# Kernel optimization log

Measured on AMD Instinct MI355X. Metric: run time of the kernel, lower is better.

The kernel has to match this reference:

```python
import jax, jax.numpy as jnp
import numpy as np

B, C, T, H, HI = 256, 64, 512, 8, 3


def setup_inputs() -> dict:
    key = jax.random.key(0)
    ks = jax.random.split(key, 20)
    s = 0.1
    return {
        "x": jax.random.normal(ks[0], (B, C, T), jnp.float32),
        "m": jax.random.uniform(ks[1], (B, C, T), jnp.float32),
        "d": jax.random.uniform(ks[2], (B, C, T), jnp.float32),
        # interpolater params (per-channel blocks of the block-diagonal matrices)
        "Wf": jax.random.normal(ks[3], (C, H, H), jnp.float32) * s,
        "Vf": jax.random.normal(ks[4], (C, H, 3), jnp.float32) * s,
        "cf": jax.random.normal(ks[5], (C, H), jnp.float32) * s,
        "Wb": jax.random.normal(ks[6], (C, H, H), jnp.float32) * s,
        "Vb": jax.random.normal(ks[7], (C, H, 3), jnp.float32) * s,
        "cb": jax.random.normal(ks[8], (C, H), jnp.float32) * s,
        "U": jax.random.normal(ks[9], (C, 2 * H), jnp.float32) * s,
        "c0": jax.random.normal(ks[10], (C,), jnp.float32) * s,
        # imputer params (nn.Linear: y = x @ W.T + b)
        "V1_w": jax.random.normal(ks[11], (HI, C), jnp.float32) * s,
        "V2_w": jax.random.normal(ks[12], (HI, C), jnp.float32) * s,
        "U_w": jax.random.normal(ks[13], (HI, C), jnp.float32) * s,
        "U_b": jax.random.normal(ks[14], (HI,), jnp.float32) * s,
        "W_w": jax.random.normal(ks[15], (C, HI), jnp.float32) * s,
        "W_b": jax.random.normal(ks[16], (C,), jnp.float32) * s,
    }


def _mrnn_forward(x, m, d, Wf, Vf, cf, Wb, Vb, cb, U, c0,
                  V1_w, V2_w, U_w, U_b, W_w, W_b):
    act = jax.nn.relu
    Bv, Cv, Tv = x.shape
    Hv = Wf.shape[-1]
    # replication pad along time: [B,C,T] -> [B,C,T+2]
    pad = lambda a: jnp.pad(a, ((0, 0), (0, 0), (1, 1)), mode='edge')
    s = jnp.stack([pad(x), pad(m), pad(d)], axis=-1)        # [B,C,T+2,3]
    # forward scan consumes padded times 0..T-1; backward consumes T+1 down to 2
    in_f = jnp.moveaxis(s[:, :, :Tv], 2, 0)                 # [T,B,C,3]
    in_b = jnp.moveaxis(s[:, :, 2:Tv + 2][:, :, ::-1], 2, 0)  # [T,B,C,3]

    def make_step(W, V, c):
        def step(h, inp):  # h:[B,C,H] inp:[B,C,3]
            hn = act(jnp.einsum('chk,bck->bch', W, h)
                     + jnp.einsum('chj,bcj->bch', V, inp) + c)
            return hn, hn
        return step

    h0 = jnp.zeros((Bv, Cv, Hv), x.dtype)
    _, hf = jax.lax.scan(make_step(Wf, Vf, cf), h0, in_f)   # [T,B,C,H]
    _, hb = jax.lax.scan(make_step(Wb, Vb, cb), h0, in_b)
    hb = hb[::-1]  # align backward hiddens with time index

    x_est = act(jnp.einsum('ch,tbch->bct', U[:, :Hv], hf)
                + jnp.einsum('ch,tbch->bct', U[:, Hv:], hb)
                + c0[None, :, None])                        # [B,C,T]

    # imputer (time as batch dim); U weight has zeroed diagonal
    idx = jnp.arange(min(U_w.shape[0], Cv))
    Uz = U_w.at[idx, idx].set(0.0)
    h = act(jnp.swapaxes(x_est, 1, 2) @ V1_w.T
            + jnp.swapaxes(m, 1, 2) @ V2_w.T
            + jnp.swapaxes(x, 1, 2) @ Uz.T + U_b)           # [B,T,HI]
    out = h @ W_w.T + W_b                                   # [B,T,C]
    return jnp.swapaxes(out, 1, 2)                          # [B,C,T]


def reference(x, m, d, Wf, Vf, cf, Wb, Vb, cb, U, c0,
              V1_w, V2_w, U_w, U_b, W_w, W_b):
    return _mrnn_forward(x, m, d, Wf, Vf, cf, Wb, Vb, cb, U, c0,
                         V1_w, V2_w, U_w, U_b, W_w, W_b)
```

## Files before the change

kernel.cpp:

```cpp
#include <hip/hip_runtime.h>

constexpr int Tn = 512;
constexpr int Cn = 64;
constexpr int Bn = 256;
constexpr int NS = 16384;

typedef float f2 __attribute__((ext_vector_type(2)));

template<int CTRL>
__device__ __forceinline__ float dppf(float v) {
    int i = __builtin_bit_cast(int, v);
    i = __builtin_amdgcn_mov_dpp(i, CTRL, 0xF, 0xF, true);
    return __builtin_bit_cast(float, i);
}

#define LDLINE(XB, MB, DB, U0) do {                                         \
    const float4* _px = (const float4*)(xp + (U0));                         \
    const float4* _pm = (const float4*)(mp + (U0));                         \
    const float4* _pd = (const float4*)(dp + (U0));                         \
    _Pragma("unroll")                                                       \
    for (int q = 0; q < 4; ++q) {                                           \
        float4 v;                                                           \
        v = _px[q]; XB[4*q]=v.x; XB[4*q+1]=v.y; XB[4*q+2]=v.z; XB[4*q+3]=v.w; \
        v = _pm[q]; MB[4*q]=v.x; MB[4*q+1]=v.y; MB[4*q+2]=v.z; MB[4*q+3]=v.w; \
        v = _pd[q]; DB[4*q]=v.x; DB[4*q+1]=v.y; DB[4*q+2]=v.z; DB[4*q+3]=v.w; \
    }                                                                       \
} while (0)

#define RUNF(XB, MB, DB, N) do {                                            \
    _Pragma("unroll")                                                       \
    for (int k = 0; k < (N); ++k) { *op = step(XB[k], MB[k], DB[k]); op += NS; } \
} while (0)

#define RUNB(XB, MB, DB, N) do {                                            \
    _Pragma("unroll")                                                       \
    for (int k = 0; k < (N); ++k) { *op = step(XB[15-k], MB[15-k], DB[15-k]); op -= NS; } \
} while (0)

__global__ __launch_bounds__(256, 2) void mrnn_scan(
    const float* __restrict__ x, const float* __restrict__ m, const float* __restrict__ d,
    const float* __restrict__ Wf, const float* __restrict__ Vf, const float* __restrict__ cf,
    const float* __restrict__ Wb, const float* __restrict__ Vb, const float* __restrict__ cbk,
    const float* __restrict__ U, float* __restrict__ accF, float* __restrict__ accB)
{
    const int g   = blockIdx.x * blockDim.x + threadIdx.x;
    const int q   = g & 3;
    const int sd  = g >> 2;
    const int dir = sd >> 14;
    const int seq = sd & 16383;
    const int c   = seq & 63;
    const long base = (long)seq * Tn;

    const float* W  = dir ? Wb  : Wf;
    const float* V  = dir ? Vb  : Vf;
    const float* cc = dir ? cbk : cf;

    const int r0 = 2 * q;
    const int r1 = 2 * q + 1;

    f2 Wp[8], Vp[3], cbp, Up;
    #pragma unroll
    for (int k = 0; k < 8; ++k) {
        Wp[k].x = W[c*64 + r0*8 + k];
        Wp[k].y = W[c*64 + r1*8 + k];
    }
    #pragma unroll
    for (int k = 0; k < 3; ++k) {
        Vp[k].x = V[c*24 + r0*3 + k];
        Vp[k].y = V[c*24 + r1*3 + k];
    }
    cbp.x = cc[c*8 + r0];  cbp.y = cc[c*8 + r1];
    Up.x  = U[c*16 + dir*8 + r0];
    Up.y  = U[c*16 + dir*8 + r1];

    f2 h = {0.f, 0.f};
    const float* xp = x + base;
    const float* mp = m + base;
    const float* dp = d + base;
    float* op = (dir ? accB : accF) + seq;

    auto step = [&](float xv, float mv, float dv) -> float {
        const float h0 = dppf<0x00>(h.x), h1 = dppf<0x00>(h.y);
        const float h2 = dppf<0x55>(h.x), h3 = dppf<0x55>(h.y);
        const float h4 = dppf<0xAA>(h.x), h5 = dppf<0xAA>(h.y);
        const float h6 = dppf<0xFF>(h.x), h7 = dppf<0xFF>(h.y);
        f2 acc = cbp;
        acc += Vp[0] * xv;
        acc += Vp[1] * mv;
        acc += Vp[2] * dv;
        acc += Wp[0] * h0;  acc += Wp[1] * h1;
        acc += Wp[2] * h2;  acc += Wp[3] * h3;
        acc += Wp[4] * h4;  acc += Wp[5] * h5;
        acc += Wp[6] * h6;  acc += Wp[7] * h7;
        acc.x = fmaxf(acc.x, 0.f);
        acc.y = fmaxf(acc.y, 0.f);
        h = acc;
        f2 dp2 = Up * acc;
        float pd = dp2.x + dp2.y;
        pd += dppf<0xB1>(pd);
        pd += dppf<0x4E>(pd);
        return pd;
    };

    float ax[16], am[16], ad[16], bx[16], bm[16], bd[16];

    if (dir == 0) {
        LDLINE(ax, am, ad, 0);
        LDLINE(bx, bm, bd, 16);
        *op = step(ax[0], am[0], ad[0]); op += NS;
        #pragma unroll 1
        for (int i = 0; i < 15; ++i) {
            RUNF(ax, am, ad, 16);
            LDLINE(ax, am, ad, 32*i + 32);
            RUNF(bx, bm, bd, 16);
            LDLINE(bx, bm, bd, 32*i + 48);
        }
        RUNF(ax, am, ad, 16);
        RUNF(bx, bm, bd, 15);
    } else {
        op += 511 * NS;
        LDLINE(ax, am, ad, 496);
        LDLINE(bx, bm, bd, 480);
        *op = step(ax[15], am[15], ad[15]); op -= NS;
        #pragma unroll 1
        for (int i = 0; i < 15; ++i) {
            RUNB(ax, am, ad, 16);
            LDLINE(ax, am, ad, 16*(29 - 2*i));
            RUNB(bx, bm, bd, 16);
            LDLINE(bx, bm, bd, 16*(28 - 2*i));
        }
        RUNB(ax, am, ad, 16);
        RUNB(bx, bm, bd, 15);
    }
}

__global__ __launch_bounds__(256, 2) void mrnn_mix(
    const float* __restrict__ x, const float* __restrict__ m,
    const float* __restrict__ accF, const float* __restrict__ accB,
    const float* __restrict__ c0, const float* __restrict__ V1w,
    const float* __restrict__ V2w, const float* __restrict__ Uw,
    const float* __restrict__ Ub, const float* __restrict__ Ww,
    const float* __restrict__ Wbias, float* __restrict__ out)
{
    const int bt = blockIdx.x * 256 + threadIdx.x;
    const int b = bt >> 9;
    const int t = bt & 511;

    const float4* aF4 = (const float4*)(accF + (size_t)t * NS + b * Cn);
    const float4* aB4 = (const float4*)(accB + (size_t)t * NS + b * Cn);
    const size_t xb = (size_t)b * (Cn * Tn) + t;

    float h0 = Ub[0], h1 = Ub[1], h2 = Ub[2];
    #pragma unroll
    for (int c4 = 0; c4 < 16; ++c4) {
        const float4 fa = aF4[c4];
        const float4 fb = aB4[c4];
        const float fav[4] = {fa.x, fa.y, fa.z, fa.w};
        const float fbv[4] = {fb.x, fb.y, fb.z, fb.w};
        #pragma unroll
        for (int j = 0; j < 4; ++j) {
            const int cch = 4*c4 + j;
            const float xe = fmaxf(fav[j] + fbv[j] + c0[cch], 0.f);
            const float mv = m[xb + (size_t)cch * Tn];
            const float xv = x[xb + (size_t)cch * Tn];
            const float u0 = (cch == 0) ? 0.f : Uw[0*Cn + cch];
            const float u1 = (cch == 1) ? 0.f : Uw[1*Cn + cch];
            const float u2 = (cch == 2) ? 0.f : Uw[2*Cn + cch];
            h0 += V1w[0*Cn + cch]*xe + V2w[0*Cn + cch]*mv + u0*xv;
            h1 += V1w[1*Cn + cch]*xe + V2w[1*Cn + cch]*mv + u1*xv;
            h2 += V1w[2*Cn + cch]*xe + V2w[2*Cn + cch]*mv + u2*xv;
        }
    }
    h0 = fmaxf(h0, 0.f); h1 = fmaxf(h1, 0.f); h2 = fmaxf(h2, 0.f);

    float* opt = out + (size_t)b * (Cn * Tn) + t;
    #pragma unroll
    for (int cch = 0; cch < Cn; ++cch) {
        opt[(size_t)cch * Tn] = Wbias[cch] + Ww[cch*3 + 0]*h0 + Ww[cch*3 + 1]*h1 + Ww[cch*3 + 2]*h2;
    }
}

extern "C" void kernel_launch(void* const* d_in, const int* in_sizes, int n_in,
                              void* d_out, int out_size, void* d_ws, size_t ws_size,
                              hipStream_t stream)
{
    const float* x   = (const float*)d_in[0];
    const float* m   = (const float*)d_in[1];
    const float* d   = (const float*)d_in[2];
    const float* Wf  = (const float*)d_in[3];
    const float* Vf  = (const float*)d_in[4];
    const float* cf  = (const float*)d_in[5];
    const float* Wb  = (const float*)d_in[6];
    const float* Vb  = (const float*)d_in[7];
    const float* cb  = (const float*)d_in[8];
    const float* U   = (const float*)d_in[9];
    const float* c0  = (const float*)d_in[10];
    const float* V1w = (const float*)d_in[11];
    const float* V2w = (const float*)d_in[12];
    const float* Uw  = (const float*)d_in[13];
    const float* Ub  = (const float*)d_in[14];
    const float* Ww  = (const float*)d_in[15];
    const float* Wb_ = (const float*)d_in[16];
    float* out = (float*)d_out;

    float* accF = (float*)d_ws;
    float* accB = accF + (size_t)Tn * NS;

    mrnn_scan<<<512, 256, 0, stream>>>(x, m, d, Wf, Vf, cf, Wb, Vb, cb, U, accF, accB);
    mrnn_mix<<<512, 256, 0, stream>>>(x, m, accF, accB, c0, V1w, V2w, Uw, Ub, Ww, Wb_, out);
}
```

Measured before the change: 114.2 us.

## Use rotating DPP broadcast and split accumulators in scan recurrence

Each quad lane now gathers the hidden state by rotating it through the quad with a single DPP rotate, three rotations per step, instead of eight separate broadcast DPP moves. The weight columns are pre-permuted per lane to match the rotation order. Two accumulator chains shorten the dependent FMA chain on the serial critical path. The input prefetch is also restructured from 16-wide register buffers to float4 double-buffering with a carried element, which cuts register pressure but shortens the prefetch distance.

```diff
diff --git a/kernel.cpp b/kernel.cpp
--- a/kernel.cpp
+++ b/kernel.cpp
@@ -2,7 +2,6 @@
 
 constexpr int Tn = 512;
 constexpr int Cn = 64;
-constexpr int Bn = 256;
 constexpr int NS = 16384;
 
 typedef float f2 __attribute__((ext_vector_type(2)));
@@ -13,28 +12,46 @@
     i = __builtin_amdgcn_mov_dpp(i, CTRL, 0xF, 0xF, true);
     return __builtin_bit_cast(float, i);
 }
-
-#define LDLINE(XB, MB, DB, U0) do {                                         \
-    const float4* _px = (const float4*)(xp + (U0));                         \
-    const float4* _pm = (const float4*)(mp + (U0));                         \
-    const float4* _pd = (const float4*)(dp + (U0));                         \
-    _Pragma("unroll")                                                       \
-    for (int q = 0; q < 4; ++q) {                                           \
-        float4 v;                                                           \
-        v = _px[q]; XB[4*q]=v.x; XB[4*q+1]=v.y; XB[4*q+2]=v.z; XB[4*q+3]=v.w; \
-        v = _pm[q]; MB[4*q]=v.x; MB[4*q+1]=v.y; MB[4*q+2]=v.z; MB[4*q+3]=v.w; \
-        v = _pd[q]; DB[4*q]=v.x; DB[4*q+1]=v.y; DB[4*q+2]=v.z; DB[4*q+3]=v.w; \
-    }                                                                       \
+__device__ __forceinline__ f2 rot1(f2 v) {
+    f2 r; r.x = dppf<0x39>(v.x); r.y = dppf<0x39>(v.y); return r;
+}
+
+#define QSTEP(xv, mv, dv, SGN) do {                                   \
+    f2 hr = h;                                                        \
+    f2 a0 = cbp + Vp0 * (xv);                                         \
+    f2 a1 = Vp1 * (mv);                                               \
+    a0 += Vp2 * (dv);                                                 \
+    a0 += WA0 * hr.x;  a1 += WB0 * hr.y;                              \
+    hr = rot1(hr);                                                    \
+    a0 += WA1 * hr.x;  a1 += WB1 * hr.y;                              \
+    hr = rot1(hr);                                                    \
+    a0 += WA2 * hr.x;  a1 += WB2 * hr.y;                              \
+    hr = rot1(hr);                                                    \
+    a0 += WA3 * hr.x;  a1 += WB3 * hr.y;                              \
+    f2 hn = a0 + a1;                                                  \
+    hn.x = fmaxf(hn.x, 0.f); hn.y = fmaxf(hn.y, 0.f);                 \
+    h = hn;                                                           \
+    float pdv = Up.x * hn.x + Up.y * hn.y;                            \
+    pdv += dppf<0xB1>(pdv);                                           \
+    pdv += dppf<0x4E>(pdv);                                           \
+    *op = pdv;                                                        \
+    op SGN NS;                                                        \
 } while (0)
 
-#define RUNF(XB, MB, DB, N) do {                                            \
-    _Pragma("unroll")                                                       \
-    for (int k = 0; k < (N); ++k) { *op = step(XB[k], MB[k], DB[k]); op += NS; } \
+#define GRP_F(X4, M4, D4) do {                                        \
+    QSTEP(cx, cm, cd, +=);                                            \
+    QSTEP((X4).x, (M4).x, (D4).x, +=);                                \
+    QSTEP((X4).y, (M4).y, (D4).y, +=);                                \
+    QSTEP((X4).z, (M4).z, (D4).z, +=);                                \
+    cx = (X4).w; cm = (M4).w; cd = (D4).w;                            \
 } while (0)
 
-#define RUNB(XB, MB, DB, N) do {                                            \
-    _Pragma("unroll")                                                       \
-    for (int k = 0; k < (N); ++k) { *op = step(XB[15-k], MB[15-k], DB[15-k]); op -= NS; } \
+#define GRP_B(X4, M4, D4) do {                                        \
+    QSTEP(cx, cm, cd, -=);                                            \
+    QSTEP((X4).w, (M4).w, (D4).w, -=);                                \
+    QSTEP((X4).z, (M4).z, (D4).z, -=);                                \
+    QSTEP((X4).y, (M4).y, (D4).y, -=);                                \
+    cx = (X4).x; cm = (M4).x; cd = (D4).x;                            \
 } while (0)
 
 __global__ __launch_bounds__(256, 2) void mrnn_scan(
@@ -55,82 +72,69 @@
     const float* V  = dir ? Vb  : Vf;
     const float* cc = dir ? cbk : cf;
 
-    const int r0 = 2 * q;
-    const int r1 = 2 * q + 1;
-
-    f2 Wp[8], Vp[3], cbp, Up;
-    #pragma unroll
-    for (int k = 0; k < 8; ++k) {
-        Wp[k].x = W[c*64 + r0*8 + k];
-        Wp[k].y = W[c*64 + r1*8 + k];
-    }
-    #pragma unroll
-    for (int k = 0; k < 3; ++k) {
-        Vp[k].x = V[c*24 + r0*3 + k];
-        Vp[k].y = V[c*24 + r1*3 + k];
-    }
-    cbp.x = cc[c*8 + r0];  cbp.y = cc[c*8 + r1];
-    Up.x  = U[c*16 + dir*8 + r0];
-    Up.y  = U[c*16 + dir*8 + r1];
+    const int r0 = 2*q, r1 = 2*q + 1;
+
+    f2 WA0, WA1, WA2, WA3, WB0, WB1, WB2, WB3, Vp0, Vp1, Vp2, cbp, Up;
+    {
+        const float* Wc = W + c*64;
+        int col;
+        col = 2*((q+0)&3);
+        WA0 = f2{Wc[r0*8+col],   Wc[r1*8+col]};
+        WB0 = f2{Wc[r0*8+col+1], Wc[r1*8+col+1]};
+        col = 2*((q+1)&3);
+        WA1 = f2{Wc[r0*8+col],   Wc[r1*8+col]};
+        WB1 = f2{Wc[r0*8+col+1], Wc[r1*8+col+1]};
+        col = 2*((q+2)&3);
+        WA2 = f2{Wc[r0*8+col],   Wc[r1*8+col]};
+        WB2 = f2{Wc[r0*8+col+1], Wc[r1*8+col+1]};
+        col = 2*((q+3)&3);
+        WA3 = f2{Wc[r0*8+col],   Wc[r1*8+col]};
+        WB3 = f2{Wc[r0*8+col+1], Wc[r1*8+col+1]};
+    }
+    Vp0 = f2{V[c*24 + r0*3 + 0], V[c*24 + r1*3 + 0]};
+    Vp1 = f2{V[c*24 + r0*3 + 1], V[c*24 + r1*3 + 1]};
+    Vp2 = f2{V[c*24 + r0*3 + 2], V[c*24 + r1*3 + 2]};
+    cbp = f2{cc[c*8 + r0], cc[c*8 + r1]};
+    Up  = f2{U[c*16 + dir*8 + r0], U[c*16 + dir*8 + r1]};
 
     f2 h = {0.f, 0.f};
-    const float* xp = x + base;
-    const float* mp = m + base;
-    const float* dp = d + base;
+    float cx, cm, cd;
+    const float4* x4 = (const float4*)(x + base);
+    const float4* m4 = (const float4*)(m + base);
+    const float4* d4 = (const float4*)(d + base);
     float* op = (dir ? accB : accF) + seq;
 
-    auto step = [&](float xv, float mv, float dv) -> float {
-        const float h0 = dppf<0x00>(h.x), h1 = dppf<0x00>(h.y);
-        const float h2 = dppf<0x55>(h.x), h3 = dppf<0x55>(h.y);
-        const float h4 = dppf<0xAA>(h.x), h5 = dppf<0xAA>(h.y);
-        const float h6 = dppf<0xFF>(h.x), h7 = dppf<0xFF>(h.y);
-        f2 acc = cbp;
-        acc += Vp[0] * xv;
-        acc += Vp[1] * mv;
-        acc += Vp[2] * dv;
-        acc += Wp[0] * h0;  acc += Wp[1] * h1;
-        acc += Wp[2] * h2;  acc += Wp[3] * h3;
-        acc += Wp[4] * h4;  acc += Wp[5] * h5;
-        acc += Wp[6] * h6;  acc += Wp[7] * h7;
-        acc.x = fmaxf(acc.x, 0.f);
-        acc.y = fmaxf(acc.y, 0.f);
-        h = acc;
-        f2 dp2 = Up * acc;
-        float pd = dp2.x + dp2.y;
-        pd += dppf<0xB1>(pd);
-        pd += dppf<0x4E>(pd);
-        return pd;
-    };
-
-    float ax[16], am[16], ad[16], bx[16], bm[16], bd[16];
-
     if (dir == 0) {
-        LDLINE(ax, am, ad, 0);
-        LDLINE(bx, bm, bd, 16);
-        *op = step(ax[0], am[0], ad[0]); op += NS;
+        float4 Ax = x4[0], Am = m4[0], Ad = d4[0];
+        float4 Bx = x4[1], Bm = m4[1], Bd = d4[1];
+        cx = Ax.x; cm = Am.x; cd = Ad.x;
         #pragma unroll 1
-        for (int i = 0; i < 15; ++i) {
-            RUNF(ax, am, ad, 16);
-            LDLINE(ax, am, ad, 32*i + 32);
-            RUNF(bx, bm, bd, 16);
-            LDLINE(bx, bm, bd, 32*i + 48);
+        for (int i = 0; i < 63; ++i) {
+            float4 Txq = x4[2*i+2], Tmq = m4[2*i+2], Tdq = d4[2*i+2];
+            GRP_F(Ax, Am, Ad);
+            float4 Uxq = x4[2*i+3], Umq = m4[2*i+3], Udq = d4[2*i+3];
+            GRP_F(Bx, Bm, Bd);
+            Ax = Txq; Am = Tmq; Ad = Tdq;
+            Bx = Uxq; Bm = Umq; Bd = Udq;
         }
-        RUNF(ax, am, ad, 16);
-        RUNF(bx, bm, bd, 15);
+        GRP_F(Ax, Am, Ad);
+        GRP_F(Bx, Bm, Bd);
     } else {
         op += 511 * NS;
-        LDLINE(ax, am, ad, 496);
-        LDLINE(bx, bm, bd, 480);
-        *op = step(ax[15], am[15], ad[15]); op -= NS;
+        float4 Ax = x4[127], Am = m4[127], Ad = d4[127];
+        float4 Bx = x4[126], Bm = m4[126], Bd = d4[126];
+        cx = Ax.w; cm = Am.w; cd = Ad.w;
         #pragma unroll 1
-        for (int i = 0; i < 15; ++i) {
-            RUNB(ax, am, ad, 16);
-            LDLINE(ax, am, ad, 16*(29 - 2*i));
-            RUNB(bx, bm, bd, 16);
-            LDLINE(bx, bm, bd, 16*(28 - 2*i));
+        for (int i = 0; i < 63; ++i) {
+            float4 Txq = x4[125-2*i], Tmq = m4[125-2*i], Tdq = d4[125-2*i];
+            GRP_B(Ax, Am, Ad);
+            float4 Uxq = x4[124-2*i], Umq = m4[124-2*i], Udq = d4[124-2*i];
+            GRP_B(Bx, Bm, Bd);
+            Ax = Txq; Am = Tmq; Ad = Tdq;
+            Bx = Uxq; Bm = Umq; Bd = Udq;
         }
-        RUNB(ax, am, ad, 16);
-        RUNB(bx, bm, bd, 15);
+        GRP_B(Ax, Am, Ad);
+        GRP_B(Bx, Bm, Bd);
     }
 }
 
```

Measured after the change: 116.8 us. 2.3% more time.

## Compute RNN recurrence steps with bf16 MFMA instead of DPP FMAs

Applied to the files above, without the earlier changes.

Each wavefront now handles 16 batch sequences for one channel and direction. Every time step becomes a single 16x16x32 bf16 MFMA, with W, V and the bias packed into the A fragment and the hidden state plus inputs packed into the B fragment. The projected outputs are stored as float4 groups of four timesteps in a new [T/4][C][B][4] workspace layout, and the mix kernel is adapted to read that layout. This is meant to cut per-step VALU and DPP work, but converting the hidden state to bf16 adds rounding error that compounds across the recurrence, and 3/4 of the matrix unit's capacity is wasted.

```diff
diff --git a/kernel.cpp b/kernel.cpp
--- a/kernel.cpp
+++ b/kernel.cpp
@@ -2,135 +2,163 @@
 
 constexpr int Tn = 512;
 constexpr int Cn = 64;
-constexpr int Bn = 256;
 constexpr int NS = 16384;
 
-typedef float f2 __attribute__((ext_vector_type(2)));
-
-template<int CTRL>
-__device__ __forceinline__ float dppf(float v) {
+typedef __attribute__((ext_vector_type(8))) short short8;
+typedef __attribute__((ext_vector_type(4))) float f32x4;
+typedef __attribute__((ext_vector_type(4))) int   i32x4;
+
+__device__ __forceinline__ unsigned cvt_pk_bf16(float lo, float hi) {
+    unsigned r;
+    asm("v_cvt_pk_bf16_f32 %0, %1, %2" : "=v"(r) : "v"(lo), "v"(hi));
+    return r;
+}
+__device__ __forceinline__ float swz_xor16(float v) {
     int i = __builtin_bit_cast(int, v);
-    i = __builtin_amdgcn_mov_dpp(i, CTRL, 0xF, 0xF, true);
+    i = __builtin_amdgcn_ds_swizzle(i, 0x401F);
     return __builtin_bit_cast(float, i);
 }
 
-#define LDLINE(XB, MB, DB, U0) do {                                         \
-    const float4* _px = (const float4*)(xp + (U0));                         \
-    const float4* _pm = (const float4*)(mp + (U0));                         \
-    const float4* _pd = (const float4*)(dp + (U0));                         \
-    _Pragma("unroll")                                                       \
-    for (int q = 0; q < 4; ++q) {                                           \
-        float4 v;                                                           \
-        v = _px[q]; XB[4*q]=v.x; XB[4*q+1]=v.y; XB[4*q+2]=v.z; XB[4*q+3]=v.w; \
-        v = _pm[q]; MB[4*q]=v.x; MB[4*q+1]=v.y; MB[4*q+2]=v.z; MB[4*q+3]=v.w; \
-        v = _pd[q]; DB[4*q]=v.x; DB[4*q+1]=v.y; DB[4*q+2]=v.z; DB[4*q+3]=v.w; \
-    }                                                                       \
+#define GRP_F(X4, M4, P4) do {                                        \
+    v0 = step(cx, cm, cd);                                            \
+    v1 = step((X4).x, (M4).x, (P4).x);                                \
+    v2 = step((X4).y, (M4).y, (P4).y);                                \
+    v3 = step((X4).z, (M4).z, (P4).z);                                \
+    if (doSt) *(float4*)op = make_float4(v0, v1, v2, v3);             \
+    op += 65536;                                                      \
+    cx = (X4).w; cm = (M4).w; cd = (P4).w;                            \
 } while (0)
 
-#define RUNF(XB, MB, DB, N) do {                                            \
-    _Pragma("unroll")                                                       \
-    for (int k = 0; k < (N); ++k) { *op = step(XB[k], MB[k], DB[k]); op += NS; } \
-} while (0)
-
-#define RUNB(XB, MB, DB, N) do {                                            \
-    _Pragma("unroll")                                                       \
-    for (int k = 0; k < (N); ++k) { *op = step(XB[15-k], MB[15-k], DB[15-k]); op -= NS; } \
+#define GRP_B(X4, M4, P4) do {                                        \
+    v3 = step(cx, cm, cd);                                            \
+    v2 = step((X4).w, (M4).w, (P4).w);                                \
+    v1 = step((X4).z, (M4).z, (P4).z);                                \
+    v0 = step((X4).y, (M4).y, (P4).y);                                \
+    if (doSt) *(float4*)op = make_float4(v0, v1, v2, v3);             \
+    op -= 65536;                                                      \
+    cx = (X4).x; cm = (M4).x; cd = (P4).x;                            \
 } while (0)
 
 __global__ __launch_bounds__(256, 2) void mrnn_scan(
     const float* __restrict__ x, const float* __restrict__ m, const float* __restrict__ d,
     const float* __restrict__ Wf, const float* __restrict__ Vf, const float* __restrict__ cf,
     const float* __restrict__ Wb, const float* __restrict__ Vb, const float* __restrict__ cbk,
-    const float* __restrict__ U, float* __restrict__ accF, float* __restrict__ accB)
+    const float* __restrict__ Uu, float* __restrict__ accF, float* __restrict__ accB)
 {
-    const int g   = blockIdx.x * blockDim.x + threadIdx.x;
-    const int q   = g & 3;
-    const int sd  = g >> 2;
-    const int dir = sd >> 14;
-    const int seq = sd & 16383;
-    const int c   = seq & 63;
-    const long base = (long)seq * Tn;
+    const int w    = blockIdx.x * 4 + (threadIdx.x >> 6);
+    const int bg   = w & 15;
+    const int c    = (w >> 4) & 63;
+    const int dir  = w >> 10;
+    const int lane = threadIdx.x & 63;
+    const int col  = lane & 15;
+    const int grp  = lane >> 4;
+    const int b    = bg * 16 + col;
 
     const float* W  = dir ? Wb  : Wf;
     const float* V  = dir ? Vb  : Vf;
     const float* cc = dir ? cbk : cf;
 
-    const int r0 = 2 * q;
-    const int r1 = 2 * q + 1;
-
-    f2 Wp[8], Vp[3], cbp, Up;
-    #pragma unroll
-    for (int k = 0; k < 8; ++k) {
-        Wp[k].x = W[c*64 + r0*8 + k];
-        Wp[k].y = W[c*64 + r1*8 + k];
-    }
-    #pragma unroll
-    for (int k = 0; k < 3; ++k) {
-        Vp[k].x = V[c*24 + r0*3 + k];
-        Vp[k].y = V[c*24 + r1*3 + k];
-    }
-    cbp.x = cc[c*8 + r0];  cbp.y = cc[c*8 + r1];
-    Up.x  = U[c*16 + dir*8 + r0];
-    Up.y  = U[c*16 + dir*8 + r1];
-
-    f2 h = {0.f, 0.f};
-    const float* xp = x + base;
-    const float* mp = m + base;
-    const float* dp = d + base;
-    float* op = (dir ? accB : accF) + seq;
+    float a0 = 0.f, a1 = 0.f, a2 = 0.f, a3 = 0.f;
+    {
+        const int row = col;
+        if (row < 8) {
+            if (grp == 0) {
+                const float* Wc = W + c*64 + row*8;
+                a0 = Wc[0]; a1 = Wc[1]; a2 = Wc[2]; a3 = Wc[3];
+            } else if (grp == 1) {
+                const float* Wc = W + c*64 + row*8;
+                a0 = Wc[4]; a1 = Wc[5]; a2 = Wc[6]; a3 = Wc[7];
+            } else if (grp == 2) {
+                a0 = V[c*24 + row*3 + 0];
+                a1 = V[c*24 + row*3 + 1];
+                a2 = V[c*24 + row*3 + 2];
+                a3 = cc[c*8 + row];
+            }
+        }
+    }
+    i32x4 ai = { (int)cvt_pk_bf16(a0, a1), (int)cvt_pk_bf16(a2, a3), 0, 0 };
+    const short8 Afrag = __builtin_bit_cast(short8, ai);
+
+    float U0 = 0.f, U1 = 0.f, U2 = 0.f, U3 = 0.f;
+    if (grp < 2) {
+        const float* Uc = Uu + c*16 + dir*8 + grp*4;
+        U0 = Uc[0]; U1 = Uc[1]; U2 = Uc[2]; U3 = Uc[3];
+    }
+
+    const bool isG2 = (grp == 2);
+    const bool isG3 = (grp == 3);
+    const bool doSt = (lane < 16);
+
+    const f32x4 z4 = {0.f, 0.f, 0.f, 0.f};
+    f32x4 hS = z4;
 
     auto step = [&](float xv, float mv, float dv) -> float {
-        const float h0 = dppf<0x00>(h.x), h1 = dppf<0x00>(h.y);
-        const float h2 = dppf<0x55>(h.x), h3 = dppf<0x55>(h.y);
-        const float h4 = dppf<0xAA>(h.x), h5 = dppf<0xAA>(h.y);
-        const float h6 = dppf<0xFF>(h.x), h7 = dppf<0xFF>(h.y);
-        f2 acc = cbp;
-        acc += Vp[0] * xv;
-        acc += Vp[1] * mv;
-        acc += Vp[2] * dv;
-        acc += Wp[0] * h0;  acc += Wp[1] * h1;
-        acc += Wp[2] * h2;  acc += Wp[3] * h3;
-        acc += Wp[4] * h4;  acc += Wp[5] * h5;
-        acc += Wp[6] * h6;  acc += Wp[7] * h7;
-        acc.x = fmaxf(acc.x, 0.f);
-        acc.y = fmaxf(acc.y, 0.f);
-        h = acc;
-        f2 dp2 = Up * acc;
-        float pd = dp2.x + dp2.y;
-        pd += dppf<0xB1>(pd);
-        pd += dppf<0x4E>(pd);
-        return pd;
+        float s0 = isG2 ? xv   : hS[0];
+        float s1 = isG2 ? mv   : hS[1];
+        float s2 = isG2 ? dv   : hS[2];
+        float s3 = isG2 ? 1.0f : hS[3];
+        unsigned b01 = cvt_pk_bf16(s0, s1);
+        unsigned b23 = cvt_pk_bf16(s2, s3);
+        b01 = isG3 ? 0u : b01;
+        b23 = isG3 ? 0u : b23;
+        i32x4 bi = { (int)b01, (int)b23, 0, 0 };
+        short8 Bfrag = __builtin_bit_cast(short8, bi);
+        f32x4 Dn = __builtin_amdgcn_mfma_f32_16x16x32_bf16(Afrag, Bfrag, z4, 0, 0, 0);
+        Dn[0] = fmaxf(Dn[0], 0.f);
+        Dn[1] = fmaxf(Dn[1], 0.f);
+        Dn[2] = fmaxf(Dn[2], 0.f);
+        Dn[3] = fmaxf(Dn[3], 0.f);
+        hS = Dn;
+        float p = U0*Dn[0] + U1*Dn[1] + U2*Dn[2] + U3*Dn[3];
+        return p + swz_xor16(p);
     };
 
-    float ax[16], am[16], ad[16], bx[16], bm[16], bd[16];
+    const float4* x4p = (const float4*)(x + ((size_t)b * Cn + c) * Tn);
+    const float4* m4p = (const float4*)(m + ((size_t)b * Cn + c) * Tn);
+    const float4* d4p = (const float4*)(d + ((size_t)b * Cn + c) * Tn);
+    float* op = (dir ? accB : accF) + c*1024 + (bg*16 + col)*4;
+
+    float cx, cm, cd, v0, v1, v2, v3;
 
     if (dir == 0) {
-        LDLINE(ax, am, ad, 0);
-        LDLINE(bx, bm, bd, 16);
-        *op = step(ax[0], am[0], ad[0]); op += NS;
+        float4 X0 = x4p[0], X1 = x4p[1], X2 = x4p[2], X3 = x4p[3];
+        float4 M0 = m4p[0], M1 = m4p[1], M2 = m4p[2], M3 = m4p[3];
+        float4 P0 = d4p[0], P1 = d4p[1], P2 = d4p[2], P3 = d4p[3];
+        cx = X0.x; cm = M0.x; cd = P0.x;
         #pragma unroll 1
-        for (int i = 0; i < 15; ++i) {
-            RUNF(ax, am, ad, 16);
-            LDLINE(ax, am, ad, 32*i + 32);
-            RUNF(bx, bm, bd, 16);
-            LDLINE(bx, bm, bd, 32*i + 48);
+        for (int i = 0; i < 31; ++i) {
+            float4 tX, tM, tP;
+            tX = x4p[4*i+4]; tM = m4p[4*i+4]; tP = d4p[4*i+4];
+            GRP_F(X0, M0, P0);  X0 = tX; M0 = tM; P0 = tP;
+            tX = x4p[4*i+5]; tM = m4p[4*i+5]; tP = d4p[4*i+5];
+            GRP_F(X1, M1, P1);  X1 = tX; M1 = tM; P1 = tP;
+            tX = x4p[4*i+6]; tM = m4p[4*i+6]; tP = d4p[4*i+6];
+            GRP_F(X2, M2, P2);  X2 = tX; M2 = tM; P2 = tP;
+            tX = x4p[4*i+7]; tM = m4p[4*i+7]; tP = d4p[4*i+7];
+            GRP_F(X3, M3, P3);  X3 = tX; M3 = tM; P3 = tP;
         }
-        RUNF(ax, am, ad, 16);
-        RUNF(bx, bm, bd, 15);
+        GRP_F(X0, M0, P0); GRP_F(X1, M1, P1);
+        GRP_F(X2, M2, P2); GRP_F(X3, M3, P3);
     } else {
-        op += 511 * NS;
-        LDLINE(ax, am, ad, 496);
-        LDLINE(bx, bm, bd, 480);
-        *op = step(ax[15], am[15], ad[15]); op -= NS;
+        op += 127 * 65536;
+        float4 X0 = x4p[127], X1 = x4p[126], X2 = x4p[125], X3 = x4p[124];
+        float4 M0 = m4p[127], M1 = m4p[126], M2 = m4p[125], M3 = m4p[124];
+        float4 P0 = d4p[127], P1 = d4p[126], P2 = d4p[125], P3 = d4p[124];
+        cx = X0.w; cm = M0.w; cd = P0.w;
         #pragma unroll 1
-        for (int i = 0; i < 15; ++i) {
-            RUNB(ax, am, ad, 16);
-            LDLINE(ax, am, ad, 16*(29 - 2*i));
-            RUNB(bx, bm, bd, 16);
-            LDLINE(bx, bm, bd, 16*(28 - 2*i));
+        for (int i = 0; i < 31; ++i) {
+            float4 tX, tM, tP;
+            tX = x4p[123-4*i]; tM = m4p[123-4*i]; tP = d4p[123-4*i];
+            GRP_B(X0, M0, P0);  X0 = tX; M0 = tM; P0 = tP;
+            tX = x4p[122-4*i]; tM = m4p[122-4*i]; tP = d4p[122-4*i];
+            GRP_B(X1, M1, P1);  X1 = tX; M1 = tM; P1 = tP;
+            tX = x4p[121-4*i]; tM = m4p[121-4*i]; tP = d4p[121-4*i];
+            GRP_B(X2, M2, P2);  X2 = tX; M2 = tM; P2 = tP;
+            tX = x4p[120-4*i]; tM = m4p[120-4*i]; tP = d4p[120-4*i];
+            GRP_B(X3, M3, P3);  X3 = tX; M3 = tM; P3 = tP;
         }
-        RUNB(ax, am, ad, 16);
-        RUNB(bx, bm, bd, 15);
+        GRP_B(X0, M0, P0); GRP_B(X1, M1, P1);
+        GRP_B(X2, M2, P2); GRP_B(X3, M3, P3);
     }
 }
 
@@ -145,31 +173,24 @@
     const int bt = blockIdx.x * 256 + threadIdx.x;
     const int b = bt >> 9;
     const int t = bt & 511;
-
-    const float4* aF4 = (const float4*)(accF + (size_t)t * NS + b * Cn);
-    const float4* aB4 = (const float4*)(accB + (size_t)t * NS + b * Cn);
+    const int tq = t >> 2, t4 = t & 3;
+
+    const float* aF = accF + (size_t)tq*65536 + b*4 + t4;
+    const float* aB = accB + (size_t)tq*65536 + b*4 + t4;
     const size_t xb = (size_t)b * (Cn * Tn) + t;
 
     float h0 = Ub[0], h1 = Ub[1], h2 = Ub[2];
-    #pragma unroll
-    for (int c4 = 0; c4 < 16; ++c4) {
-        const float4 fa = aF4[c4];
-        const float4 fb = aB4[c4];
-        const float fav[4] = {fa.x, fa.y, fa.z, fa.w};
-        const float fbv[4] = {fb.x, fb.y, fb.z, fb.w};
-        #pragma unroll
-        for (int j = 0; j < 4; ++j) {
-            const int cch = 4*c4 + j;
-            const float xe = fmaxf(fav[j] + fbv[j] + c0[cch], 0.f);
-            const float mv = m[xb + (size_t)cch * Tn];
-            const float xv = x[xb + (size_t)cch * Tn];
-            const float u0 = (cch == 0) ? 0.f : Uw[0*Cn + cch];
-            const float u1 = (cch == 1) ? 0.f : Uw[1*Cn + cch];
-            const float u2 = (cch == 2) ? 0.f : Uw[2*Cn + cch];
-            h0 += V1w[0*Cn + cch]*xe + V2w[0*Cn + cch]*mv + u0*xv;
-            h1 += V1w[1*Cn + cch]*xe + V2w[1*Cn + cch]*mv + u1*xv;
-            h2 += V1w[2*Cn + cch]*xe + V2w[2*Cn + cch]*mv + u2*xv;
-        }
+    #pragma unroll 16
+    for (int cch = 0; cch < Cn; ++cch) {
+        const float xe = fmaxf(aF[cch*1024] + aB[cch*1024] + c0[cch], 0.f);
+        const float mv = m[xb + (size_t)cch * Tn];
+        const float xv = x[xb + (size_t)cch * Tn];
+        const float u0 = (cch == 0) ? 0.f : Uw[0*Cn + cch];
+        const float u1 = (cch == 1) ? 0.f : Uw[1*Cn + cch];
+        const float u2 = (cch == 2) ? 0.f : Uw[2*Cn + cch];
+        h0 += V1w[0*Cn + cch]*xe + V2w[0*Cn + cch]*mv + u0*xv;
+        h1 += V1w[1*Cn + cch]*xe + V2w[1*Cn + cch]*mv + u1*xv;
+        h2 += V1w[2*Cn + cch]*xe + V2w[2*Cn + cch]*mv + u2*xv;
     }
     h0 = fmaxf(h0, 0.f); h1 = fmaxf(h1, 0.f); h2 = fmaxf(h2, 0.f);
 
```

New measurement: 162.7 us. 1.43x slower.
